# Performance work log

Measured on AMD Instinct MI355X. Metric: run time of the kernel, lower is better.

The kernel has to match this reference:

```python
import jax, jax.numpy as jnp
import numpy as np

DIM = 512
HEADS = 8
DIM_HEAD = 64
INNER = HEADS * DIM_HEAD  # 512
SCALE = DIM_HEAD ** -0.5
NEG = -jnp.finfo(jnp.float32).max


def setup_inputs() -> dict:
    key = jax.random.key(0)
    k1, k2, k3, k4, k5 = jax.random.split(key, 5)
    b, n = 2, 4096
    x = jax.random.normal(k1, (b, n, DIM), dtype=jnp.float32)
    mask = jnp.ones((b, n), dtype=bool)
    gamma = jnp.ones((DIM,), dtype=jnp.float32)
    # nn.Linear default init ~ U(-1/sqrt(fan_in), 1/sqrt(fan_in)); use scaled normal for simplicity
    Wq = jax.random.normal(k2, (DIM, INNER), dtype=jnp.float32) * (DIM ** -0.5)
    Wkv = jax.random.normal(k3, (DIM, 2 * INNER), dtype=jnp.float32) * (DIM ** -0.5)
    Wout = jax.random.normal(k4, (INNER, DIM), dtype=jnp.float32) * (INNER ** -0.5)
    return {"x": x, "mask": mask, "gamma": gamma, "Wq": Wq, "Wkv": Wkv, "Wout": Wout}


def _layer_norm(x, gamma):
    mu = jnp.mean(x, axis=-1, keepdims=True)
    var = jnp.var(x, axis=-1, keepdims=True)
    return (x - mu) * jax.lax.rsqrt(var + 1e-5) * gamma  # beta buffer is zeros


def reference(x, mask, gamma, Wq, Wkv, Wout):
    b, n, _ = x.shape
    xn = _layer_norm(x, gamma)
    q = xn @ Wq                      # [b,n,inner]
    kv = xn @ Wkv                    # [b,n,2*inner]
    k, v = jnp.split(kv, 2, axis=-1)
    # b n (h d) -> b h n d
    def split_heads(t):
        return t.reshape(b, n, HEADS, DIM_HEAD).transpose(0, 2, 1, 3)
    q, k, v = split_heads(q) * SCALE, split_heads(k), split_heads(v)
    sim = jnp.einsum('bhid,bhjd->bhij', q, k)  # [b,h,n,n]
    sim = jnp.where(mask[:, None, None, :], sim, NEG)
    causal = jnp.triu(jnp.ones((n, n), dtype=bool), k=1)
    sim = jnp.where(causal, NEG, sim)
    attn = jax.nn.softmax(sim, axis=-1)
    out = jnp.einsum('bhij,bhjd->bhid', attn, v)       # [b,h,n,d]
    out = out.transpose(0, 2, 1, 3).reshape(b, n, INNER)
    return out @ Wout
```

## Files before the change

### kernel.cpp

```cpp
#include <hip/hip_runtime.h>
#include <hip/hip_bf16.h>
#include <stdint.h>

typedef __attribute__((ext_vector_type(8))) short bf16x8;
typedef __attribute__((ext_vector_type(4))) float f32x4;
typedef __attribute__((ext_vector_type(16))) float f32x16;
typedef __attribute__((ext_vector_type(4))) uint32_t u32x4;

__device__ __forceinline__ short f2bf(float f) {
    union { float f; uint32_t u; } v; v.f = f;
    uint32_t r = v.u + 0x7fffu + ((v.u >> 16) & 1u);
    return (short)(r >> 16);
}

__device__ __forceinline__ uint32_t cvtpk(float a, float b) {
    uint32_t r;
    asm("v_cvt_pk_bf16_f32 %0, %1, %2" : "=v"(r) : "v"(a), "v"(b));
    return r;
}

__device__ __forceinline__ void plswap(uint32_t& x, uint32_t& y) {
    asm volatile("v_permlane32_swap_b32 %0, %1" : "+v"(x), "+v"(y));
}

__device__ __forceinline__ f32x16 mfma32(bf16x8 a, bf16x8 b, f32x16 c) {
    return __builtin_amdgcn_mfma_f32_32x32x16_bf16(a, b, c, 0, 0, 0);
}

__device__ __forceinline__ void gload_lds16(const void* g, void* l) {
    __builtin_amdgcn_global_load_lds(
        (const __attribute__((address_space(1))) void*)g,
        (__attribute__((address_space(3))) void*)l, 16, 0, 0);
}

__global__ __launch_bounds__(256) void prep_weights(
    const float* __restrict__ Wq, const float* __restrict__ Wkv,
    const float* __restrict__ Wout, short* __restrict__ WqkvT,
    short* __restrict__ WoutT) {
    int tid = blockIdx.x * 256 + threadIdx.x;
    if (tid < 1536 * 512) {
        int n = tid >> 9, k = tid & 511;
        float w = (n < 512) ? Wq[k * 512 + n] : Wkv[k * 1024 + (n - 512)];
        WqkvT[tid] = f2bf(w);
    } else {
        int t = tid - 1536 * 512;
        int n = t >> 9, k = t & 511;
        WoutT[t] = f2bf(Wout[k * 512 + n]);
    }
}

__global__ __launch_bounds__(256) void layernorm_k(
    const float* __restrict__ x, const float* __restrict__ gamma,
    short* __restrict__ xn) {
    int row = blockIdx.x;
    const float* xr = x + (size_t)row * 512;
    float2 v = *(const float2*)(xr + threadIdx.x * 2);
    float s = v.x + v.y;
    float ss = v.x * v.x + v.y * v.y;
#pragma unroll
    for (int off = 1; off < 64; off <<= 1) {
        s += __shfl_xor(s, off);
        ss += __shfl_xor(ss, off);
    }
    __shared__ float sbuf[4], ssbuf[4];
    int wid = threadIdx.x >> 6;
    if ((threadIdx.x & 63) == 0) { sbuf[wid] = s; ssbuf[wid] = ss; }
    __syncthreads();
    s = sbuf[0] + sbuf[1] + sbuf[2] + sbuf[3];
    ss = ssbuf[0] + ssbuf[1] + ssbuf[2] + ssbuf[3];
    float mu = s * (1.f / 512.f);
    float var = ss * (1.f / 512.f) - mu * mu;
    float rstd = rsqrtf(var + 1e-5f);
    float2 g = *(const float2*)(gamma + threadIdx.x * 2);
    uint32_t lo = (uint16_t)f2bf((v.x - mu) * rstd * g.x);
    uint32_t hi = (uint16_t)f2bf((v.y - mu) * rstd * g.y);
    *(uint32_t*)(xn + (size_t)row * 512 + threadIdx.x * 2) = lo | (hi << 16);
}

template <int EPI>
__global__ __launch_bounds__(256) void gemm_bt(const short* __restrict__ A,
                                               const short* __restrict__ Bt,
                                               void* __restrict__ C) {
    constexpr int K = 512;
    constexpr int CS = (EPI == 0) ? 1536 : 512;
    __shared__ __align__(16) short As[128 * 64];
    __shared__ __align__(16) short Bs[128 * 64];
    const int tid = threadIdx.x;
    const int lane = tid & 63;
    const int wid = tid >> 6;
    const int m0 = blockIdx.x * 128;
    const int n0 = blockIdx.y * 128;
    const int wr = wid >> 1, wc = wid & 1;
    const int hi = lane >> 4, lo = lane & 15;

    f32x4 acc[4][4] = {};
    for (int kt = 0; kt < K / 64; ++kt) {
        __syncthreads();
#pragma unroll
        for (int r = 0; r < 4; ++r) {
            int c = (r * 4 + wid) * 64 + lane;
            int row = c >> 3, c8 = c & 7;
            int kcol = kt * 64 + ((c8 ^ (row & 7)) << 3);
            gload_lds16(A + (size_t)(m0 + row) * K + kcol,
                        (char*)As + (r * 4 + wid) * 1024);
            gload_lds16(Bt + (size_t)(n0 + row) * K + kcol,
                        (char*)Bs + (r * 4 + wid) * 1024);
        }
        __syncthreads();
#pragma unroll
        for (int kk = 0; kk < 2; ++kk) {
            bf16x8 af[4], bfr[4];
            int cc = hi + kk * 4;
#pragma unroll
            for (int i = 0; i < 4; ++i) {
                int row = wr * 64 + i * 16 + lo;
                af[i] = *(const bf16x8*)((const char*)As + row * 128 +
                                         ((cc ^ (row & 7)) << 4));
                int nrow = wc * 64 + i * 16 + lo;
                bfr[i] = *(const bf16x8*)((const char*)Bs + nrow * 128 +
                                          ((cc ^ (nrow & 7)) << 4));
            }
#pragma unroll
            for (int i = 0; i < 4; ++i)
#pragma unroll
                for (int j = 0; j < 4; ++j)
                    acc[i][j] = __builtin_amdgcn_mfma_f32_16x16x32_bf16(
                        af[i], bfr[j], acc[i][j], 0, 0, 0);
        }
    }
#pragma unroll
    for (int i = 0; i < 4; ++i)
#pragma unroll
        for (int j = 0; j < 4; ++j) {
            int col = n0 + wc * 64 + j * 16 + lo;
#pragma unroll
            for (int r = 0; r < 4; ++r) {
                int row = m0 + wr * 64 + i * 16 + hi * 4 + r;
                float v = acc[i][j][r];
                if (EPI == 0) {
                    if (col < 512) v *= 0.18033688011112042f;
                    ((short*)C)[(size_t)row * CS + col] = f2bf(v);
                } else {
                    ((float*)C)[(size_t)row * CS + col] = v;
                }
            }
        }
}

__global__ __launch_bounds__(256) void transpose_v(const short* __restrict__ qkv,
                                                   short* __restrict__ Vt) {
    __shared__ __align__(16) short T[64 * 72];
    int tid = threadIdx.x;
    int bh = blockIdx.y, b = bh >> 3, h = bh & 7;
    int n0 = blockIdx.x * 64;
    const short* src = qkv + (size_t)(b * 4096 + n0) * 1536 + 1024 + h * 64;
#pragma unroll
    for (int r = 0; r < 2; ++r) {
        int c = r * 256 + tid;
        int t = c >> 3, d0 = (c & 7) * 8;
        *(bf16x8*)(&T[t * 72 + d0]) = *(const bf16x8*)(src + (size_t)t * 1536 + d0);
    }
    __syncthreads();
    short* dst = Vt + (size_t)bh * 64 * 4096 + n0;
#pragma unroll
    for (int r = 0; r < 2; ++r) {
        int c = r * 256 + tid;
        int d = c >> 3, tt0 = (c & 7) * 8;
        short o[8];
#pragma unroll
        for (int j = 0; j < 8; ++j) o[j] = T[(tt0 + j) * 72 + d];
        *(bf16x8*)(dst + (size_t)d * 4096 + tt0) = *(bf16x8*)o;
    }
}

__global__ __launch_bounds__(256, 2) void flash_attn(
    const short* __restrict__ qkv, const short* __restrict__ Vt,
    short* __restrict__ attn_out) {
    __shared__ __align__(16) char smem[65536];
    const int tid = threadIdx.x, lane = tid & 63, w = tid >> 6;
    const int hi32 = lane >> 5, lq = lane & 31;
    const int bid = blockIdx.x;
    const int qt = 127 - (bid >> 4);
    const int bh = bid & 15, b = bh >> 3, h = bh & 7;
    const int q0 = qt * 32;
    const int qg = q0 + lq;
    const int swz = (lq & 7) ^ ((lq >> 3) & 1);

    bf16x8 qb[4];
    {
        const short* qrow = qkv + (size_t)(b * 4096 + qg) * 1536 + h * 64;
#pragma unroll
        for (int ks = 0; ks < 4; ++ks)
            qb[ks] = *(const bf16x8*)(qrow + ks * 16 + hi32 * 8);
    }

    const short* kptr = qkv + (size_t)b * 4096 * 1536 + 512 + h * 64;
    const short* vptr = Vt + (size_t)bh * 64 * 4096;
    char* mybuf = smem + w * 16384;

    auto stage = [&](int t) {
        const short* kp = kptr + (size_t)t * 64 * 1536;
        const short* vp = vptr + t * 64;
#pragma unroll
        for (int r = 0; r < 8; ++r) {
            int idx = r * 64 + lane;
            int row = idx >> 3, c = idx & 7;
            int sw = (row & 7) ^ ((row >> 3) & 1);
            gload_lds16(kp + (size_t)row * 1536 + ((c ^ sw) << 3),
                        mybuf + r * 1024);
            gload_lds16(vp + (size_t)row * 4096 + ((c ^ sw) << 3),
                        mybuf + 8192 + r * 1024);
        }
    };

    f32x16 oA = {}, oB = {};
    float m_r = -3.0e38f, l_r = 0.f;
    const int T = (q0 + 31) / 64 + 1;

    if (w < T) {
        stage(w);
        for (int t = w; t < T; t += 4) {
            asm volatile("s_waitcnt vmcnt(0)" ::: "memory");
            f32x16 sA = {}, sB = {};
            __builtin_amdgcn_s_setprio(1);
#pragma unroll
            for (int ks = 0; ks < 4; ++ks) {
                int p = (2 * ks + hi32) ^ swz;
                bf16x8 kfA = *(const bf16x8*)(mybuf + lq * 128 + p * 16);
                bf16x8 kfB = *(const bf16x8*)(mybuf + (lq + 32) * 128 + p * 16);
                sA = mfma32(kfA, qb[ks], sA);
                sB = mfma32(kfB, qb[ks], sB);
            }
            __builtin_amdgcn_s_setprio(0);
            bf16x8 vfA[4], vfB[4];
#pragma unroll
            for (int ks = 0; ks < 4; ++ks) {
                int p = (2 * ks + hi32) ^ swz;
                vfA[ks] = *(const bf16x8*)(mybuf + 8192 + lq * 128 + p * 16);
                vfB[ks] = *(const bf16x8*)(mybuf + 8192 + (lq + 32) * 128 + p * 16);
            }
            asm volatile("s_waitcnt lgkmcnt(0)" ::: "memory");
            __builtin_amdgcn_sched_barrier(0);
            if (t + 4 < T) stage(t + 4);
            int kv0 = t * 64;
            if (kv0 + 63 > q0) {
                int c4 = 4 * hi32;
#pragma unroll
                for (int r2 = 0; r2 < 16; ++r2) {
                    int kvl = (r2 & 3) + 8 * (r2 >> 2) + c4;
                    sA[r2] = (kv0 + kvl > qg) ? -3.0e38f : sA[r2];
                    sB[r2] = (kv0 + 32 + kvl > qg) ? -3.0e38f : sB[r2];
                }
            }
            float m0 = m_r, m1 = m_r, m2 = m_r, m3 = m_r;
#pragma unroll
            for (int r2 = 0; r2 < 16; r2 += 4) {
                m0 = fmaxf(fmaxf(sA[r2], sB[r2]), m0);
                m1 = fmaxf(fmaxf(sA[r2 + 1], sB[r2 + 1]), m1);
                m2 = fmaxf(fmaxf(sA[r2 + 2], sB[r2 + 2]), m2);
                m3 = fmaxf(fmaxf(sA[r2 + 3], sB[r2 + 3]), m3);
            }
            float mt = fmaxf(fmaxf(m0, m1), fmaxf(m2, m3));
            mt = fmaxf(mt, __shfl_xor(mt, 32));
            if (!__all(mt <= m_r + 8.0f)) {
                float alpha = exp2f(m_r - mt);
                m_r = mt;
                l_r *= alpha;
#pragma unroll
                for (int r2 = 0; r2 < 16; ++r2) {
                    oA[r2] *= alpha;
                    oB[r2] *= alpha;
                }
            }
            float sum0 = 0.f, sum1 = 0.f;
#pragma unroll
            for (int r2 = 0; r2 < 16; ++r2) {
                sA[r2] = exp2f(sA[r2] - m_r);
                sB[r2] = exp2f(sB[r2] - m_r);
                sum0 += sA[r2];
                sum1 += sB[r2];
            }
            float rs = sum0 + sum1;
            rs += __shfl_xor(rs, 32);
            l_r += rs;
#pragma unroll
            for (int ks = 0; ks < 4; ++ks) {
                const int base = (ks & 1) * 8;
                float e0, e1, e2, e3, e4, e5, e6, e7;
                if (ks < 2) {
                    e0 = sA[base + 0]; e1 = sA[base + 1]; e2 = sA[base + 2];
                    e3 = sA[base + 3]; e4 = sA[base + 4]; e5 = sA[base + 5];
                    e6 = sA[base + 6]; e7 = sA[base + 7];
                } else {
                    e0 = sB[base + 0]; e1 = sB[base + 1]; e2 = sB[base + 2];
                    e3 = sB[base + 3]; e4 = sB[base + 4]; e5 = sB[base + 5];
                    e6 = sB[base + 6]; e7 = sB[base + 7];
                }
                uint32_t x0 = cvtpk(e0, e1), y0 = cvtpk(e4, e5);
                plswap(x0, y0);
                uint32_t x1 = cvtpk(e2, e3), y1 = cvtpk(e6, e7);
                plswap(x1, y1);
                union { uint32_t wd[4]; bf16x8 v; } u;
                u.wd[0] = x0; u.wd[1] = x1; u.wd[2] = y0; u.wd[3] = y1;
                __builtin_amdgcn_s_setprio(1);
                oA = mfma32(vfA[ks], u.v, oA);
                oB = mfma32(vfB[ks], u.v, oB);
                __builtin_amdgcn_s_setprio(0);
            }
        }
    }
    __syncthreads();
    float* Ocmb = (float*)smem;
    float* mlb = (float*)(smem + 34816);
#pragma unroll
    for (int g = 0; g < 4; ++g) {
        f32x4 a = {oA[4 * g], oA[4 * g + 1], oA[4 * g + 2], oA[4 * g + 3]};
        f32x4 bq = {oB[4 * g], oB[4 * g + 1], oB[4 * g + 2], oB[4 * g + 3]};
        int d0 = 8 * g + 4 * hi32;
        *(f32x4*)(Ocmb + (w * 32 + lq) * 68 + d0) = a;
        *(f32x4*)(Ocmb + (w * 32 + lq) * 68 + 32 + d0) = bq;
    }
    if (hi32 == 0) {
        mlb[w * 64 + lq] = m_r;
        mlb[w * 64 + 32 + lq] = l_r;
    }
    __syncthreads();
    {
        const int q = tid >> 3, dg = tid & 7;
        float M = -3.0e38f;
        float mm[4], ll[4];
#pragma unroll
        for (int s = 0; s < 4; ++s) {
            mm[s] = mlb[s * 64 + q];
            ll[s] = mlb[s * 64 + 32 + q];
            M = fmaxf(M, mm[s]);
        }
        float L = 0.f;
        float acc[8] = {};
#pragma unroll
        for (int s = 0; s < 4; ++s) {
            float a = exp2f(mm[s] - M);
            L += a * ll[s];
            const float* Os = Ocmb + (s * 32 + q) * 68 + dg * 8;
            f32x4 lo = *(const f32x4*)Os;
            f32x4 hi = *(const f32x4*)(Os + 4);
#pragma unroll
            for (int j = 0; j < 4; ++j) {
                acc[j] += a * lo[j];
                acc[4 + j] += a * hi[j];
            }
        }
        float inv = 1.0f / L;
        u32x4 o;
#pragma unroll
        for (int j = 0; j < 4; ++j)
            o[j] = cvtpk(acc[2 * j] * inv, acc[2 * j + 1] * inv);
        uint32_t* attn32 = (uint32_t*)attn_out;
        *(u32x4*)(attn32 + (size_t)(b * 4096 + q0 + q) * 256 + h * 32 + dg * 4) = o;
    }
}

extern "C" void kernel_launch(void* const* d_in, const int* in_sizes, int n_in,
                              void* d_out, int out_size, void* d_ws,
                              size_t ws_size, hipStream_t stream) {
    const float* x = (const float*)d_in[0];
    const float* gamma = (const float*)d_in[2];
    const float* Wq = (const float*)d_in[3];
    const float* Wkv = (const float*)d_in[4];
    const float* Wout = (const float*)d_in[5];

    char* ws = (char*)d_ws;
    short* xn = (short*)(ws);
    short* qkv = (short*)(ws + (8ull << 20));
    short* Vt = (short*)(ws + (32ull << 20));
    short* attn = (short*)(ws + (40ull << 20));
    short* WqkvT = (short*)(ws + (48ull << 20));
    short* WoutT = (short*)(ws + (50ull << 20));

    prep_weights<<<4096, 256, 0, stream>>>(Wq, Wkv, Wout, WqkvT, WoutT);
    layernorm_k<<<8192, 256, 0, stream>>>(x, gamma, xn);
    gemm_bt<0><<<dim3(64, 12), 256, 0, stream>>>(xn, WqkvT, qkv);
    transpose_v<<<dim3(64, 16), 256, 0, stream>>>(qkv, Vt);
    flash_attn<<<2048, 256, 0, stream>>>(qkv, Vt, attn);
    gemm_bt<1><<<dim3(64, 4), 256, 0, stream>>>(attn, WoutT, (float*)d_out);
}
```

Baseline: 137.7 us.

## Halve KV tile to 32 and shared memory to raise flash-attention occupancy

Shrinks each wave's KV tile from 64 to 32 keys, halving per-wave LDS staging and dropping the second score accumulator, so the kernel can run 4 blocks per CU instead of 2. V tiles get a new swizzle for the 32-wide rows. The epilogue now stores per-wave normalized partial outputs as bf16 in shared memory, which shrinks the combine buffer and changes the merge weights to use l. The cost is twice as many loop iterations with more per-tile overhead (waitcnts, max/shuffle, rescale checks) and some extra rounding in the combine.

```diff
diff --git a/kernel.cpp b/kernel.cpp
--- a/kernel.cpp
+++ b/kernel.cpp
@@ -11,6 +11,11 @@
     union { float f; uint32_t u; } v; v.f = f;
     uint32_t r = v.u + 0x7fffu + ((v.u >> 16) & 1u);
     return (short)(r >> 16);
+}
+
+__device__ __forceinline__ float bf2f(uint32_t bits) {
+    union { uint32_t u; float f; } v; v.u = bits;
+    return v.f;
 }
 
 __device__ __forceinline__ uint32_t cvtpk(float a, float b) {
@@ -173,10 +178,10 @@
     }
 }
 
-__global__ __launch_bounds__(256, 2) void flash_attn(
+__global__ __launch_bounds__(256, 4) void flash_attn(
     const short* __restrict__ qkv, const short* __restrict__ Vt,
     short* __restrict__ attn_out) {
-    __shared__ __align__(16) char smem[65536];
+    __shared__ __align__(16) char smem[32768];
     const int tid = threadIdx.x, lane = tid & 63, w = tid >> 6;
     const int hi32 = lane >> 5, lq = lane & 31;
     const int bid = blockIdx.x;
@@ -184,7 +189,8 @@
     const int bh = bid & 15, b = bh >> 3, h = bh & 7;
     const int q0 = qt * 32;
     const int qg = q0 + lq;
-    const int swz = (lq & 7) ^ ((lq >> 3) & 1);
+    const int swzK = (lq & 7) ^ ((lq >> 3) & 1);
+    const int swzV = (lq >> 1) & 3;
 
     bf16x8 qb[4];
     {
@@ -196,69 +202,69 @@
 
     const short* kptr = qkv + (size_t)b * 4096 * 1536 + 512 + h * 64;
     const short* vptr = Vt + (size_t)bh * 64 * 4096;
-    char* mybuf = smem + w * 16384;
+    char* mybuf = smem + w * 8192;
 
     auto stage = [&](int t) {
-        const short* kp = kptr + (size_t)t * 64 * 1536;
-        const short* vp = vptr + t * 64;
-#pragma unroll
-        for (int r = 0; r < 8; ++r) {
+        const short* kp = kptr + (size_t)t * 32 * 1536;
+        const short* vp = vptr + t * 32;
+#pragma unroll
+        for (int r = 0; r < 4; ++r) {
             int idx = r * 64 + lane;
-            int row = idx >> 3, c = idx & 7;
-            int sw = (row & 7) ^ ((row >> 3) & 1);
-            gload_lds16(kp + (size_t)row * 1536 + ((c ^ sw) << 3),
-                        mybuf + r * 1024);
-            gload_lds16(vp + (size_t)row * 4096 + ((c ^ sw) << 3),
-                        mybuf + 8192 + r * 1024);
+            int krow = idx >> 3, kc = idx & 7;
+            int ksw = (krow & 7) ^ ((krow >> 3) & 1);
+            gload_lds16(kp + (size_t)krow * 1536 + ((kc ^ ksw) << 3),
+                        mybuf + idx * 16);
+            int vrow = idx >> 2, vc = idx & 3;
+            int vcl = vc ^ ((vrow >> 1) & 3);
+            gload_lds16(vp + (size_t)vrow * 4096 + (vcl << 3),
+                        mybuf + 4096 + idx * 16);
         }
     };
 
     f32x16 oA = {}, oB = {};
     float m_r = -3.0e38f, l_r = 0.f;
-    const int T = (q0 + 31) / 64 + 1;
+    const int T = qt + 1;
 
     if (w < T) {
         stage(w);
         for (int t = w; t < T; t += 4) {
             asm volatile("s_waitcnt vmcnt(0)" ::: "memory");
-            f32x16 sA = {}, sB = {};
+            f32x16 sA = {};
             __builtin_amdgcn_s_setprio(1);
 #pragma unroll
             for (int ks = 0; ks < 4; ++ks) {
-                int p = (2 * ks + hi32) ^ swz;
-                bf16x8 kfA = *(const bf16x8*)(mybuf + lq * 128 + p * 16);
-                bf16x8 kfB = *(const bf16x8*)(mybuf + (lq + 32) * 128 + p * 16);
-                sA = mfma32(kfA, qb[ks], sA);
-                sB = mfma32(kfB, qb[ks], sB);
+                int p = (2 * ks + hi32) ^ swzK;
+                bf16x8 kf = *(const bf16x8*)(mybuf + lq * 128 + p * 16);
+                sA = mfma32(kf, qb[ks], sA);
             }
             __builtin_amdgcn_s_setprio(0);
-            bf16x8 vfA[4], vfB[4];
-#pragma unroll
-            for (int ks = 0; ks < 4; ++ks) {
-                int p = (2 * ks + hi32) ^ swz;
-                vfA[ks] = *(const bf16x8*)(mybuf + 8192 + lq * 128 + p * 16);
-                vfB[ks] = *(const bf16x8*)(mybuf + 8192 + (lq + 32) * 128 + p * 16);
+            bf16x8 vfA[2], vfB[2];
+#pragma unroll
+            for (int ks = 0; ks < 2; ++ks) {
+                int p = (2 * ks + hi32) ^ swzV;
+                vfA[ks] = *(const bf16x8*)(mybuf + 4096 + lq * 64 + p * 16);
+                vfB[ks] =
+                    *(const bf16x8*)(mybuf + 4096 + (lq + 32) * 64 + p * 16);
             }
             asm volatile("s_waitcnt lgkmcnt(0)" ::: "memory");
             __builtin_amdgcn_sched_barrier(0);
             if (t + 4 < T) stage(t + 4);
-            int kv0 = t * 64;
-            if (kv0 + 63 > q0) {
+            int kv0 = t * 32;
+            if (kv0 + 31 > q0) {
                 int c4 = 4 * hi32;
 #pragma unroll
                 for (int r2 = 0; r2 < 16; ++r2) {
                     int kvl = (r2 & 3) + 8 * (r2 >> 2) + c4;
                     sA[r2] = (kv0 + kvl > qg) ? -3.0e38f : sA[r2];
-                    sB[r2] = (kv0 + 32 + kvl > qg) ? -3.0e38f : sB[r2];
                 }
             }
             float m0 = m_r, m1 = m_r, m2 = m_r, m3 = m_r;
 #pragma unroll
             for (int r2 = 0; r2 < 16; r2 += 4) {
-                m0 = fmaxf(fmaxf(sA[r2], sB[r2]), m0);
-                m1 = fmaxf(fmaxf(sA[r2 + 1], sB[r2 + 1]), m1);
-                m2 = fmaxf(fmaxf(sA[r2 + 2], sB[r2 + 2]), m2);
-                m3 = fmaxf(fmaxf(sA[r2 + 3], sB[r2 + 3]), m3);
+                m0 = fmaxf(sA[r2], m0);
+                m1 = fmaxf(sA[r2 + 1], m1);
+                m2 = fmaxf(sA[r2 + 2], m2);
+                m3 = fmaxf(sA[r2 + 3], m3);
             }
             float mt = fmaxf(fmaxf(m0, m1), fmaxf(m2, m3));
             mt = fmaxf(mt, __shfl_xor(mt, 32));
@@ -272,33 +278,22 @@
                     oB[r2] *= alpha;
                 }
             }
-            float sum0 = 0.f, sum1 = 0.f;
+            float sum0 = 0.f;
 #pragma unroll
             for (int r2 = 0; r2 < 16; ++r2) {
                 sA[r2] = exp2f(sA[r2] - m_r);
-                sB[r2] = exp2f(sB[r2] - m_r);
                 sum0 += sA[r2];
-                sum1 += sB[r2];
-            }
-            float rs = sum0 + sum1;
-            rs += __shfl_xor(rs, 32);
+            }
+            float rs = sum0 + __shfl_xor(sum0, 32);
             l_r += rs;
 #pragma unroll
-            for (int ks = 0; ks < 4; ++ks) {
-                const int base = (ks & 1) * 8;
-                float e0, e1, e2, e3, e4, e5, e6, e7;
-                if (ks < 2) {
-                    e0 = sA[base + 0]; e1 = sA[base + 1]; e2 = sA[base + 2];
-                    e3 = sA[base + 3]; e4 = sA[base + 4]; e5 = sA[base + 5];
-                    e6 = sA[base + 6]; e7 = sA[base + 7];
-                } else {
-                    e0 = sB[base + 0]; e1 = sB[base + 1]; e2 = sB[base + 2];
-                    e3 = sB[base + 3]; e4 = sB[base + 4]; e5 = sB[base + 5];
-                    e6 = sB[base + 6]; e7 = sB[base + 7];
-                }
-                uint32_t x0 = cvtpk(e0, e1), y0 = cvtpk(e4, e5);
+            for (int ks = 0; ks < 2; ++ks) {
+                const int base = ks * 8;
+                uint32_t x0 = cvtpk(sA[base + 0], sA[base + 1]);
+                uint32_t y0 = cvtpk(sA[base + 4], sA[base + 5]);
                 plswap(x0, y0);
-                uint32_t x1 = cvtpk(e2, e3), y1 = cvtpk(e6, e7);
+                uint32_t x1 = cvtpk(sA[base + 2], sA[base + 3]);
+                uint32_t y1 = cvtpk(sA[base + 6], sA[base + 7]);
                 plswap(x1, y1);
                 union { uint32_t wd[4]; bf16x8 v; } u;
                 u.wd[0] = x0; u.wd[1] = x1; u.wd[2] = y0; u.wd[3] = y1;
@@ -310,23 +305,27 @@
         }
     }
     __syncthreads();
-    float* Ocmb = (float*)smem;
-    float* mlb = (float*)(smem + 34816);
-#pragma unroll
-    for (int g = 0; g < 4; ++g) {
-        f32x4 a = {oA[4 * g], oA[4 * g + 1], oA[4 * g + 2], oA[4 * g + 3]};
-        f32x4 bq = {oB[4 * g], oB[4 * g + 1], oB[4 * g + 2], oB[4 * g + 3]};
-        int d0 = 8 * g + 4 * hi32;
-        *(f32x4*)(Ocmb + (w * 32 + lq) * 68 + d0) = a;
-        *(f32x4*)(Ocmb + (w * 32 + lq) * 68 + 32 + d0) = bq;
-    }
-    if (hi32 == 0) {
-        mlb[w * 64 + lq] = m_r;
-        mlb[w * 64 + 32 + lq] = l_r;
+    {
+        char* epi = smem + w * 4352;
+        float invl = (l_r > 0.f) ? (1.0f / l_r) : 0.f;
+#pragma unroll
+        for (int r2 = 0; r2 < 16; r2 += 2) {
+            int wbase = ((r2 & 3) >> 1) + 4 * (r2 >> 2) + 2 * hi32;
+            *(uint32_t*)(epi + lq * 136 + wbase * 4) =
+                cvtpk(oA[r2] * invl, oA[r2 + 1] * invl);
+            *(uint32_t*)(epi + lq * 136 + 64 + wbase * 4) =
+                cvtpk(oB[r2] * invl, oB[r2 + 1] * invl);
+        }
+        float* mlb = (float*)(smem + 17408);
+        if (hi32 == 0) {
+            mlb[w * 64 + lq] = m_r;
+            mlb[w * 64 + 32 + lq] = l_r;
+        }
     }
     __syncthreads();
     {
         const int q = tid >> 3, dg = tid & 7;
+        const float* mlb = (const float*)(smem + 17408);
         float M = -3.0e38f;
         float mm[4], ll[4];
 #pragma unroll
@@ -339,15 +338,13 @@
         float acc[8] = {};
 #pragma unroll
         for (int s = 0; s < 4; ++s) {
-            float a = exp2f(mm[s] - M);
-            L += a * ll[s];
-            const float* Os = Ocmb + (s * 32 + q) * 68 + dg * 8;
-            f32x4 lo = *(const f32x4*)Os;
-            f32x4 hi = *(const f32x4*)(Os + 4);
+            float a = exp2f(mm[s] - M) * ll[s];
+            L += a;
+            u32x4 pv = *(const u32x4*)(smem + s * 4352 + q * 136 + dg * 16);
 #pragma unroll
             for (int j = 0; j < 4; ++j) {
-                acc[j] += a * lo[j];
-                acc[4 + j] += a * hi[j];
+                acc[2 * j] += a * bf2f(pv[j] << 16);
+                acc[2 * j + 1] += a * bf2f(pv[j] & 0xffff0000u);
             }
         }
         float inv = 1.0f / L;
@@ -356,7 +353,8 @@
         for (int j = 0; j < 4; ++j)
             o[j] = cvtpk(acc[2 * j] * inv, acc[2 * j + 1] * inv);
         uint32_t* attn32 = (uint32_t*)attn_out;
-        *(u32x4*)(attn32 + (size_t)(b * 4096 + q0 + q) * 256 + h * 32 + dg * 4) = o;
+        *(u32x4*)(attn32 + (size_t)(b * 4096 + q0 + q) * 256 + h * 32 + dg * 4) =
+            o;
     }
 }
 
```

Measured after the change: 133.7 us. 1.03x faster.
